# Optimization experiments

Measured on AMD Instinct MI355X. Metric: run time of the kernel, lower is better.

The kernel has to match this reference:

```python
import jax, jax.numpy as jnp
import numpy as np

DIM = 192
NUM_HEADS = 8
EPS = 1e-12  # F.normalize default eps


def setup_inputs() -> dict:
    key = jax.random.key(0)
    ks = jax.random.split(key, 6)
    b, c, h, w = 8, DIM, 128, 128
    scale = 1.0 / np.sqrt(DIM)  # conv2d default init scale (approx)
    return {
        "input": jax.random.normal(ks[0], (b, c, h, w), dtype=jnp.float32),
        "color": jax.random.normal(ks[1], (b, c, h, w), dtype=jnp.float32),
        "Wq": jax.random.normal(ks[2], (DIM, DIM), dtype=jnp.float32) * scale,
        "Wk": jax.random.normal(ks[3], (DIM, DIM), dtype=jnp.float32) * scale,
        "Wv": jax.random.normal(ks[4], (DIM, DIM), dtype=jnp.float32) * scale,
        "Wo": jax.random.normal(ks[5], (DIM, DIM), dtype=jnp.float32) * scale,
    }


def _proj(x, W):
    # 1x1 conv (bias=False) == channel GEMM: [b,c,h,w] x [out,c] -> [b,out,h,w]
    return jnp.einsum('bchw,oc->bohw', x, W)


def _l2norm(x):
    n = jnp.sqrt(jnp.sum(x * x, axis=-1, keepdims=True))
    return x / jnp.maximum(n, EPS)


def reference(input, color, Wq, Wk, Wv, Wo):
    b, c, h, w = input.shape
    head = NUM_HEADS
    dh = c // head
    hw = h * w
    # q from color, k/v from input
    q = _proj(color, Wq).reshape(b, head, dh, hw)
    k = _proj(input, Wk).reshape(b, head, dh, hw)
    v = _proj(input, Wv).reshape(b, head, dh, hw)
    q = _l2norm(q)
    k = _l2norm(k)
    # transposed (channel) attention: [b,head,dh,dh]
    attn = jnp.einsum('bhcn,bhdn->bhcd', q, k)
    attn = jax.nn.softmax(attn, axis=-1)
    out = jnp.einsum('bhcd,bhdn->bhcn', attn, v)  # [b,head,dh,hw]
    out = out.reshape(b, c, h, w)
    return _proj(out, Wo)
```

## Files before the change

### kernel.cpp

```cpp
#include <hip/hip_runtime.h>
#include <hip/hip_bf16.h>


typedef __attribute__((ext_vector_type(4))) float f32x4;
typedef __attribute__((ext_vector_type(8))) short short8;

#define MFMA16(a, b, c) __builtin_amdgcn_mfma_f32_16x16x32_bf16((a), (b), (c), 0, 0, 0)

__device__ __forceinline__ unsigned int pack_rne(float a, float b) {
  unsigned int ua = __float_as_uint(a), ub = __float_as_uint(b);
  ua += 0x7fffu + ((ua >> 16) & 1u);
  ub += 0x7fffu + ((ub >> 16) & 1u);
  return (ua >> 16) | (ub & 0xffff0000u);
}
__device__ __forceinline__ unsigned short bf16u_rne(float x) {
  unsigned int u = __float_as_uint(x);
  u += 0x7fffu + ((u >> 16) & 1u);
  return (unsigned short)(u >> 16);
}
union S8U { short8 s; unsigned int u[4]; };
__device__ __forceinline__ short8 load_cvt8(const float* p) {
  f32x4 x = *(const f32x4*)p;
  f32x4 y = *(const f32x4*)(p + 4);
  S8U r;
  r.u[0] = pack_rne(x[0], x[1]);
  r.u[1] = pack_rne(x[2], x[3]);
  r.u[2] = pack_rne(y[0], y[1]);
  r.u[3] = pack_rne(y[2], y[3]);
  return r.s;
}

#define HW 16384
#define CDIM 192
#define NB 8
#define GSZ (CDIM * CDIM)
#define NTILE 300
#define FCHUNK 49152
#define BROW 80

__global__ void k0_wvt(const float* __restrict__ Wv, unsigned short* __restrict__ WvT) {
  int idx = blockIdx.x * 256 + threadIdx.x;
  if (idx < CDIM * CDIM) {
    int j = idx / CDIM, cp = idx % CDIM;
    WvT[idx] = bf16u_rne(Wv[(size_t)cp * CDIM + j]);
  }
}

__device__ __forceinline__ short8 bfrag(const char* buf, int row, int lg) {
  return *(const short8*)(buf + row * BROW + lg * 16);
}

__device__ __forceinline__ void stageF(const float* __restrict__ ib,
                                       const float* __restrict__ cb, int c0,
                                       char* fdst, int wave, int lane) {
#pragma unroll
  for (int i = 0; i < 4; ++i) {
    const int instr = wave * 4 + i;
    const int tensor = instr >= 24;
    const int rl = (instr - (tensor ? 24 : 0)) * 8 + (lane >> 3);
    const float* T = tensor ? cb : ib;
    const float* g = T + (size_t)rl * HW + c0 + (lane & 7) * 4;
    __builtin_amdgcn_global_load_lds(
        (const __attribute__((address_space(1))) void*)g,
        (__attribute__((address_space(3))) void*)(fdst + instr * 1024), 16, 0, 0);
  }
}

template <int W>
__device__ __forceinline__ void pair_step(const char* bb, f32x4 (&acc)[25],
                                          int l15, int lg) {
  const short8 aT = bfrag(bb, W * 16 + l15, lg);
  const short8 aB = bfrag(bb, (23 - W) * 16 + l15, lg);
#pragma unroll
  for (int ct = W; ct < 24; ++ct) {
    const short8 b = bfrag(bb, ct * 16 + l15, lg);
    acc[ct - W] = MFMA16(aT, b, acc[ct - W]);
    if (ct >= 23 - W) acc[ct + 1] = MFMA16(aB, b, acc[ct + 1]);
  }
}

__device__ __forceinline__ void pair_dispatch(int wave, const char* bb,
                                              f32x4 (&acc)[25], int l15, int lg) {
  switch (wave) {
    case 0: pair_step<0>(bb, acc, l15, lg); break;
    case 1: pair_step<1>(bb, acc, l15, lg); break;
    case 2: pair_step<2>(bb, acc, l15, lg); break;
    case 3: pair_step<3>(bb, acc, l15, lg); break;
    case 4: pair_step<4>(bb, acc, l15, lg); break;
    case 5: pair_step<5>(bb, acc, l15, lg); break;
    case 6: pair_step<6>(bb, acc, l15, lg); break;
    case 7: pair_step<7>(bb, acc, l15, lg); break;
    case 8: pair_step<8>(bb, acc, l15, lg); break;
    case 9: pair_step<9>(bb, acc, l15, lg); break;
    case 10: pair_step<10>(bb, acc, l15, lg); break;
    default: pair_step<11>(bb, acc, l15, lg); break;
  }
}

__global__ __launch_bounds__(768) void gram2_k(const float* __restrict__ input,
                                               const float* __restrict__ color,
                                               float* __restrict__ part,
                                               int npart, int cpb) {
  __shared__ __align__(16) char fbuf[2][FCHUNK];
  __shared__ __align__(16) char bbuf[384 * BROW];
  const int tid = threadIdx.x, wave = tid >> 6, lane = tid & 63;
  const int l15 = lane & 15, lg = (lane >> 4) & 3;
  const int strip = blockIdx.x, b = blockIdx.y;
  const float* ib = input + (size_t)b * CDIM * HW;
  const float* cb = color + (size_t)b * CDIM * HW;
  const int cbase = strip * cpb;

  f32x4 acc[25];
#pragma unroll
  for (int i = 0; i < 25; ++i) acc[i] = (f32x4){0.f, 0.f, 0.f, 0.f};

  stageF(ib, cb, cbase * 32, fbuf[0], wave, lane);
#pragma unroll 1
  for (int c = 0; c < cpb; ++c) {
    if (c + 1 < cpb) {
      stageF(ib, cb, (cbase + c + 1) * 32, fbuf[(c + 1) & 1], wave, lane);
      asm volatile("s_waitcnt vmcnt(4)" ::: "memory");
    } else {
      asm volatile("s_waitcnt vmcnt(0)" ::: "memory");
    }
    __builtin_amdgcn_sched_barrier(0);
    __builtin_amdgcn_s_barrier();
    {
      const char* fb = fbuf[c & 1];
#pragma unroll
      for (int u0 = 0; u0 < 2; ++u0) {
        const int u = tid + u0 * 768;
        const int zr = u >> 2, sub = u & 3;
        const char* src = fb + zr * 128 + sub * 32;
        f32x4 x = *(const f32x4*)src;
        f32x4 y = *(const f32x4*)(src + 16);
        S8U pk;
        pk.u[0] = pack_rne(x[0], x[1]);
        pk.u[1] = pack_rne(x[2], x[3]);
        pk.u[2] = pack_rne(y[0], y[1]);
        pk.u[3] = pack_rne(y[2], y[3]);
        *(short8*)(bbuf + zr * BROW + sub * 16) = pk.s;
      }
    }
    asm volatile("s_waitcnt lgkmcnt(0)" ::: "memory");
    __builtin_amdgcn_sched_barrier(0);
    __builtin_amdgcn_s_barrier();
    pair_dispatch(wave, bbuf, acc, l15, lg);
  }

  float* pbase = part + (size_t)(b * npart + strip) * NTILE * 256;
#pragma unroll
  for (int s = 0; s < 25; ++s)
    *(f32x4*)(pbase + ((size_t)(wave * 25 + s) * 64 + lane) * 4) = acc[s];
}

template <int NP>
__global__ __launch_bounds__(256) void reduce_k(const float* __restrict__ part,
                                                float* __restrict__ G) {
  const int b = blockIdx.y;
  const int T = blockIdx.x * 4 + (threadIdx.x >> 6);
  const int lane = threadIdx.x & 63;
  const float* p = part + ((size_t)b * NP * NTILE + T) * 256 + lane * 4;
  f32x4 v[NP];
#pragma unroll
  for (int s = 0; s < NP; ++s) v[s] = *(const f32x4*)(p + (size_t)s * NTILE * 256);
  f32x4 sum = v[0];
#pragma unroll
  for (int s = 1; s < NP; ++s) {
    sum[0] += v[s][0]; sum[1] += v[s][1]; sum[2] += v[s][2]; sum[3] += v[s][3];
  }
  const int w = T / 25, s = T % 25;
  int rt, ct;
  if (s <= 23 - w) { rt = w; ct = w + s; }
  else { rt = 23 - w; ct = s - 1; }
  int type, gm, gn;
  if (ct < 12) { type = 2; gm = rt; gn = ct; }
  else if (rt < 12) { type = 0; gm = rt; gn = ct - 12; }
  else { type = 1; gm = rt - 12; gn = ct - 12; }
  float* Gm = G + ((size_t)type * NB + b) * GSZ;
  const int l15 = lane & 15, lg = lane >> 4;
  const int row0 = gm * 16 + lg * 4, col = gn * 16 + l15;
#pragma unroll
  for (int r = 0; r < 4; ++r) Gm[(size_t)(row0 + r) * CDIM + col] = sum[r];
  if (type != 0 && rt != ct) {
#pragma unroll
    for (int r = 0; r < 4; ++r) Gm[(size_t)col * CDIM + (row0 + r)] = sum[r];
  }
}

__global__ __launch_bounds__(256) void k2a(const float* __restrict__ G,
                                           const float* __restrict__ Wq,
                                           const float* __restrict__ Wk,
                                           float* __restrict__ A_pre,
                                           float* __restrict__ nqk) {
  const int b = blockIdx.x, type = blockIdx.y;
  __shared__ __align__(16) unsigned short Hs[192][200];
  const int tid = threadIdx.x, wave = tid >> 6, lane = tid & 63;
  const int l15 = lane & 15, lg = lane >> 4, row0 = wave * 48;
  const float* W1 = (type == 2) ? Wk : Wq;
  const float* Gm = G + ((size_t)type * NB + b) * GSZ;

  f32x4 acc[3][12];
#pragma unroll
  for (int t = 0; t < 3; t++)
#pragma unroll
    for (int j = 0; j < 12; j++) acc[t][j] = (f32x4){0.f, 0.f, 0.f, 0.f};

  for (int ks = 0; ks < 192; ks += 32) {
    short8 afr[3];
#pragma unroll
    for (int t = 0; t < 3; t++)
      afr[t] = load_cvt8(W1 + (size_t)(row0 + t * 16 + l15) * CDIM + ks + lg * 8);
#pragma unroll
    for (int tj = 0; tj < 12; tj++) {
      short8 bfr = load_cvt8(Gm + (size_t)(tj * 16 + l15) * CDIM + ks + lg * 8);
#pragma unroll
      for (int t = 0; t < 3; t++) acc[t][tj] = MFMA16(afr[t], bfr, acc[t][tj]);
    }
  }
#pragma unroll
  for (int t = 0; t < 3; t++)
#pragma unroll
    for (int tj = 0; tj < 12; tj++)
#pragma unroll
      for (int r = 0; r < 4; r++)
        Hs[row0 + t * 16 + lg * 4 + r][tj * 16 + l15] = bf16u_rne(acc[t][tj][r]);
  __syncthreads();

  if (type == 0) {
    f32x4 a2[3][12];
#pragma unroll
    for (int t = 0; t < 3; t++)
#pragma unroll
      for (int j = 0; j < 12; j++) a2[t][j] = (f32x4){0.f, 0.f, 0.f, 0.f};
    for (int ks = 0; ks < 192; ks += 32) {
      short8 afr[3];
#pragma unroll
      for (int t = 0; t < 3; t++)
        afr[t] = *(const short8*)&Hs[row0 + t * 16 + l15][ks + lg * 8];
#pragma unroll
      for (int tj = 0; tj < 12; tj++) {
        short8 bfr = load_cvt8(Wk + (size_t)(tj * 16 + l15) * CDIM + ks + lg * 8);
#pragma unroll
        for (int t = 0; t < 3; t++) a2[t][tj] = MFMA16(afr[t], bfr, a2[t][tj]);
      }
    }
    float* Ab = A_pre + (size_t)b * GSZ;
#pragma unroll
    for (int t = 0; t < 3; t++)
#pragma unroll
      for (int tj = 0; tj < 12; tj++)
#pragma unroll
        for (int r = 0; r < 4; r++)
          Ab[(size_t)(row0 + t * 16 + lg * 4 + r) * CDIM + tj * 16 + l15] = a2[t][tj][r];
  } else {
    f32x4 a2[3];
#pragma unroll
    for (int t = 0; t < 3; t++) a2[t] = (f32x4){0.f, 0.f, 0.f, 0.f};
    for (int ks = 0; ks < 192; ks += 32) {
#pragma unroll
      for (int t = 0; t < 3; t++) {
        short8 afr = *(const short8*)&Hs[row0 + t * 16 + l15][ks + lg * 8];
        short8 bfr = load_cvt8(W1 + (size_t)(row0 + t * 16 + l15) * CDIM + ks + lg * 8);
        a2[t] = MFMA16(afr, bfr, a2[t]);
      }
    }
    float* dst = nqk + ((size_t)(type - 1) * NB + b) * CDIM;
#pragma unroll
    for (int t = 0; t < 3; t++)
#pragma unroll
      for (int r = 0; r < 4; r++)
        if (lg * 4 + r == l15) dst[row0 + t * 16 + l15] = a2[t][r];
  }
}

__global__ void k2b(const float* __restrict__ A_pre, const float* __restrict__ nqk,
                    float* __restrict__ attnw) {
  const int b = blockIdx.x, tid = threadIdx.x;
  const int h = tid >> 5, r = tid & 31;
  if (r >= 24) return;
  const float* Ab = A_pre + (size_t)b * GSZ;
  const float* nq = nqk + (size_t)b * CDIM;
  const float* nk = nqk + (size_t)(NB + b) * CDIM;
  const int c = h * 24 + r;
  const float qn = rsqrtf(fmaxf(nq[c], 1e-24f));
  float e[24];
  float mx = -1e30f;
#pragma unroll
  for (int d = 0; d < 24; d++) {
    float kn = rsqrtf(fmaxf(nk[h * 24 + d], 1e-24f));
    float l = Ab[(size_t)c * CDIM + h * 24 + d] * qn * kn;
    e[d] = l;
    mx = fmaxf(mx, l);
  }
  float s = 0.f;
#pragma unroll
  for (int d = 0; d < 24; d++) {
    float x = __expf(e[d] - mx);
    e[d] = x;
    s += x;
  }
  const float inv = 1.0f / s;
  float* dst = attnw + (((size_t)b * NB + h) * 24 + r) * 24;
#pragma unroll
  for (int d = 0; d < 24; d++) dst[d] = e[d] * inv;
}

__global__ __launch_bounds__(256) void k3(const float* __restrict__ attnw,
                                          const float* __restrict__ Wo,
                                          const unsigned short* __restrict__ WvT,
                                          unsigned short* __restrict__ Pbf) {
  const int b = blockIdx.x;
  __shared__ __align__(16) unsigned short AT[192][200];
  __shared__ __align__(16) unsigned short Ms[192][200];
  const int tid = threadIdx.x, wave = tid >> 6, lane = tid & 63;
  const int l15 = lane & 15, lg = lane >> 4, row0 = wave * 48;

  unsigned int* ATu = (unsigned int*)&AT[0][0];
  for (int i = tid; i < 192 * 100; i += 256) ATu[i] = 0u;
  __syncthreads();
  const float* at = attnw + (size_t)b * NB * 24 * 24;
  for (int i = tid; i < 4608; i += 256) {
    int h = i / 576, rem = i % 576, c = rem / 24, d = rem % 24;
    AT[h * 24 + d][h * 24 + c] = bf16u_rne(at[(h * 24 + c) * 24 + d]);
  }
  __syncthreads();

  f32x4 acc[3][12];
#pragma unroll
  for (int t = 0; t < 3; t++)
#pragma unroll
    for (int j = 0; j < 12; j++) acc[t][j] = (f32x4){0.f, 0.f, 0.f, 0.f};
  for (int ks = 0; ks < 192; ks += 32) {
    short8 afr[3];
#pragma unroll
    for (int t = 0; t < 3; t++)
      afr[t] = load_cvt8(Wo + (size_t)(row0 + t * 16 + l15) * CDIM + ks + lg * 8);
#pragma unroll
    for (int tj = 0; tj < 12; tj++) {
      short8 bfr = *(const short8*)&AT[tj * 16 + l15][ks + lg * 8];
#pragma unroll
      for (int t = 0; t < 3; t++) acc[t][tj] = MFMA16(afr[t], bfr, acc[t][tj]);
    }
  }
#pragma unroll
  for (int t = 0; t < 3; t++)
#pragma unroll
    for (int tj = 0; tj < 12; tj++)
#pragma unroll
      for (int r = 0; r < 4; r++)
        Ms[row0 + t * 16 + lg * 4 + r][tj * 16 + l15] = bf16u_rne(acc[t][tj][r]);
  __syncthreads();

  f32x4 a2[3][12];
#pragma unroll
  for (int t = 0; t < 3; t++)
#pragma unroll
    for (int j = 0; j < 12; j++) a2[t][j] = (f32x4){0.f, 0.f, 0.f, 0.f};
  for (int ks = 0; ks < 192; ks += 32) {
    short8 afr[3];
#pragma unroll
    for (int t = 0; t < 3; t++)
      afr[t] = *(const short8*)&Ms[row0 + t * 16 + l15][ks + lg * 8];
#pragma unroll
    for (int tj = 0; tj < 12; tj++) {
      short8 bfr = *(const short8*)(WvT + (size_t)(tj * 16 + l15) * CDIM + ks + lg * 8);
#pragma unroll
      for (int t = 0; t < 3; t++) a2[t][tj] = MFMA16(afr[t], bfr, a2[t][tj]);
    }
  }
  unsigned short* Pb = Pbf + (size_t)b * GSZ;
#pragma unroll
  for (int t = 0; t < 3; t++)
#pragma unroll
    for (int tj = 0; tj < 12; tj++)
#pragma unroll
      for (int r = 0; r < 4; r++)
        Pb[(size_t)(row0 + t * 16 + lg * 4 + r) * CDIM + tj * 16 + l15] = bf16u_rne(a2[t][tj][r]);
}

__global__ __launch_bounds__(256) void kD(const unsigned short* __restrict__ Pbf,
                                          const float* __restrict__ input,
                                          float* __restrict__ out) {
  const int nchunk = blockIdx.x, b = blockIdx.y;
  const int n0 = nchunk * 128;
  __shared__ __align__(16) char BsT[128 * 384];
  const int tid = threadIdx.x, wave = tid >> 6, lane = tid & 63;
  const int l15 = lane & 15, lg = lane >> 4, row0 = wave * 48;

  {
    const int n4 = (tid & 31) * 4;
    const int kb0 = (tid >> 5) * 4;
    const float* src = input + (size_t)b * CDIM * HW + n0 + n4;
    f32x4 w[24];
#pragma unroll
    for (int rnd = 0; rnd < 6; ++rnd)
#pragma unroll
      for (int j = 0; j < 4; ++j)
        w[rnd * 4 + j] = *(const f32x4*)(src + (size_t)(kb0 + rnd * 32 + j) * HW);
    __builtin_amdgcn_sched_barrier(0);
    char* bsb = BsT;
#pragma unroll
    for (int rnd = 0; rnd < 6; ++rnd) {
      const int kb = kb0 + rnd * 32;
#pragma unroll
      for (int i = 0; i < 4; ++i) {
        const int n = n4 + i;
        unsigned long long pk =
            (unsigned long long)pack_rne(w[rnd * 4 + 0][i], w[rnd * 4 + 1][i]) |
            ((unsigned long long)pack_rne(w[rnd * 4 + 2][i], w[rnd * 4 + 3][i]) << 32);
        *(unsigned long long*)(bsb + n * 384 + ((kb * 2) ^ ((n & 7) << 4))) = pk;
      }
    }
  }
  __syncthreads();

  f32x4 acc[3][8];
#pragma unroll
  for (int t = 0; t < 3; t++)
#pragma unroll
    for (int j = 0; j < 8; j++) acc[t][j] = (f32x4){0.f, 0.f, 0.f, 0.f};

  const unsigned short* Pb = Pbf + (size_t)b * GSZ;
#pragma unroll 2
  for (int ks = 0; ks < 6; ks++) {
    short8 afr[3];
#pragma unroll
    for (int t = 0; t < 3; t++)
      afr[t] = *(const short8*)(Pb + (size_t)(row0 + t * 16 + l15) * CDIM + ks * 32 + lg * 8);
#pragma unroll
    for (int tn = 0; tn < 8; tn++) {
      const int n = tn * 16 + l15;
      short8 bfr = *(const short8*)(BsT + n * 384 + ((ks * 64 + lg * 16) ^ ((n & 7) << 4)));
#pragma unroll
      for (int t = 0; t < 3; t++) acc[t][tn] = MFMA16(afr[t], bfr, acc[t][tn]);
    }
  }
  float* ob = out + (size_t)b * CDIM * HW + n0;
#pragma unroll
  for (int t = 0; t < 3; t++)
#pragma unroll
    for (int tn = 0; tn < 8; tn++)
#pragma unroll
      for (int r = 0; r < 4; r++) {
        const int m = row0 + t * 16 + lg * 4 + r;
        ob[(size_t)m * HW + tn * 16 + l15] = acc[t][tn][r];
      }
}

extern "C" void kernel_launch(void* const* d_in, const int* in_sizes, int n_in,
                              void* d_out, int out_size, void* d_ws, size_t ws_size,
                              hipStream_t stream) {
  const float* input = (const float*)d_in[0];
  const float* color = (const float*)d_in[1];
  const float* Wq = (const float*)d_in[2];
  const float* Wk = (const float*)d_in[3];
  const float* Wv = (const float*)d_in[4];
  const float* Wo = (const float*)d_in[5];
  float* out = (float*)d_out;
  char* ws = (char*)d_ws;

  const size_t OFF_G = 0;
  const size_t OFF_APRE = 3538944;
  const size_t OFF_NQK = OFF_APRE + 1179648;
  const size_t OFF_ATT = OFF_NQK + 12288;
  const size_t OFF_WVT = OFF_ATT + 147456;
  const size_t OFF_PBF = OFF_WVT + 73728;
  const size_t OFF_PART = OFF_PBF + 589824;

  float* G = (float*)(ws + OFF_G);
  float* A_pre = (float*)(ws + OFF_APRE);
  float* nqk = (float*)(ws + OFF_NQK);
  float* attnw = (float*)(ws + OFF_ATT);
  unsigned short* WvT = (unsigned short*)(ws + OFF_WVT);
  unsigned short* Pbf = (unsigned short*)(ws + OFF_PBF);
  float* part = (float*)(ws + OFF_PART);

  int npart = 32;
  while (npart > 2 && OFF_PART + (size_t)npart * NB * NTILE * 1024 > ws_size) npart >>= 1;
  const int cpb = 512 / npart;

  k0_wvt<<<dim3(144), dim3(256), 0, stream>>>(Wv, WvT);
  gram2_k<<<dim3(npart, NB), dim3(768), 0, stream>>>(input, color, part, npart, cpb);
  switch (npart) {
    case 32: reduce_k<32><<<dim3(75, NB), dim3(256), 0, stream>>>(part, G); break;
    case 16: reduce_k<16><<<dim3(75, NB), dim3(256), 0, stream>>>(part, G); break;
    case 8:  reduce_k<8><<<dim3(75, NB), dim3(256), 0, stream>>>(part, G); break;
    case 4:  reduce_k<4><<<dim3(75, NB), dim3(256), 0, stream>>>(part, G); break;
    default: reduce_k<2><<<dim3(75, NB), dim3(256), 0, stream>>>(part, G); break;
  }
  k2a<<<dim3(NB, 3), dim3(256), 0, stream>>>(G, Wq, Wk, A_pre, nqk);
  k2b<<<dim3(NB), dim3(256), 0, stream>>>(A_pre, nqk, attnw);
  k3<<<dim3(NB), dim3(256), 0, stream>>>(attnw, Wo, WvT, Pbf);
  kD<<<dim3(HW / 128, NB), dim3(256), 0, stream>>>(Pbf, input, out);
}
```

Measured before the change: 203.5 us.

## Deepen gram staging pipeline to four 16-column slots with prefetch after barrier

The Gram kernel now splits each 32-column chunk into two 16-column slots (64-byte row segments) held in a four-slot LDS ring. It prefetches two chunks ahead, issuing those loads after the conversion barrier so the slots being overwritten are no longer read. The aim is to keep more global loads in flight and hide memory latency behind the MFMA work. The cost is shorter contiguous row segments per load and a vmcnt(4) wait that now relies on the new issue order.

```diff
diff --git a/kernel.cpp b/kernel.cpp
--- a/kernel.cpp
+++ b/kernel.cpp
@@ -35,7 +35,7 @@
 #define NB 8
 #define GSZ (CDIM * CDIM)
 #define NTILE 300
-#define FCHUNK 49152
+#define FSLOT 24576
 #define BROW 80
 
 __global__ void k0_wvt(const float* __restrict__ Wv, unsigned short* __restrict__ WvT) {
@@ -50,19 +50,19 @@
   return *(const short8*)(buf + row * BROW + lg * 16);
 }
 
-__device__ __forceinline__ void stageF(const float* __restrict__ ib,
-                                       const float* __restrict__ cb, int c0,
+__device__ __forceinline__ void stageC(const float* __restrict__ ib,
+                                       const float* __restrict__ cb, int col0,
                                        char* fdst, int wave, int lane) {
 #pragma unroll
-  for (int i = 0; i < 4; ++i) {
-    const int instr = wave * 4 + i;
-    const int tensor = instr >= 24;
-    const int rl = (instr - (tensor ? 24 : 0)) * 8 + (lane >> 3);
+  for (int i = 0; i < 2; ++i) {
+    const int g = wave * 2 + i;
+    const int tensor = g >= 12;
+    const int row = (g - (tensor ? 12 : 0)) * 16 + (lane >> 2);
     const float* T = tensor ? cb : ib;
-    const float* g = T + (size_t)rl * HW + c0 + (lane & 7) * 4;
+    const float* gp = T + (size_t)row * HW + col0 + (lane & 3) * 4;
     __builtin_amdgcn_global_load_lds(
-        (const __attribute__((address_space(1))) void*)g,
-        (__attribute__((address_space(3))) void*)(fdst + instr * 1024), 16, 0, 0);
+        (const __attribute__((address_space(1))) void*)gp,
+        (__attribute__((address_space(3))) void*)(fdst + g * 1024), 16, 0, 0);
   }
 }
 
@@ -100,25 +100,28 @@
 __global__ __launch_bounds__(768) void gram2_k(const float* __restrict__ input,
                                                const float* __restrict__ color,
                                                float* __restrict__ part,
-                                               int npart, int cpb) {
-  __shared__ __align__(16) char fbuf[2][FCHUNK];
+                                               int npart, int ncp) {
+  __shared__ __align__(16) char fbuf[4][FSLOT];
   __shared__ __align__(16) char bbuf[384 * BROW];
   const int tid = threadIdx.x, wave = tid >> 6, lane = tid & 63;
   const int l15 = lane & 15, lg = (lane >> 4) & 3;
   const int strip = blockIdx.x, b = blockIdx.y;
   const float* ib = input + (size_t)b * CDIM * HW;
   const float* cb = color + (size_t)b * CDIM * HW;
-  const int cbase = strip * cpb;
+  const int ch0 = strip * ncp * 2;
 
   f32x4 acc[25];
 #pragma unroll
   for (int i = 0; i < 25; ++i) acc[i] = (f32x4){0.f, 0.f, 0.f, 0.f};
 
-  stageF(ib, cb, cbase * 32, fbuf[0], wave, lane);
+  stageC(ib, cb, (ch0 + 0) * 16, fbuf[0], wave, lane);
+  stageC(ib, cb, (ch0 + 1) * 16, fbuf[1], wave, lane);
+  stageC(ib, cb, (ch0 + 2) * 16, fbuf[2], wave, lane);
+  stageC(ib, cb, (ch0 + 3) * 16, fbuf[3], wave, lane);
+
 #pragma unroll 1
-  for (int c = 0; c < cpb; ++c) {
-    if (c + 1 < cpb) {
-      stageF(ib, cb, (cbase + c + 1) * 32, fbuf[(c + 1) & 1], wave, lane);
+  for (int cp = 0; cp < ncp; ++cp) {
+    if (cp + 1 < ncp) {
       asm volatile("s_waitcnt vmcnt(4)" ::: "memory");
     } else {
       asm volatile("s_waitcnt vmcnt(0)" ::: "memory");
@@ -126,12 +129,13 @@
     __builtin_amdgcn_sched_barrier(0);
     __builtin_amdgcn_s_barrier();
     {
-      const char* fb = fbuf[c & 1];
+      const char* sA = fbuf[(2 * cp) & 3];
+      const char* sB = fbuf[(2 * cp + 1) & 3];
 #pragma unroll
       for (int u0 = 0; u0 < 2; ++u0) {
         const int u = tid + u0 * 768;
         const int zr = u >> 2, sub = u & 3;
-        const char* src = fb + zr * 128 + sub * 32;
+        const char* src = (sub < 2 ? sA : sB) + zr * 64 + (sub & 1) * 32;
         f32x4 x = *(const f32x4*)src;
         f32x4 y = *(const f32x4*)(src + 16);
         S8U pk;
@@ -145,6 +149,10 @@
     asm volatile("s_waitcnt lgkmcnt(0)" ::: "memory");
     __builtin_amdgcn_sched_barrier(0);
     __builtin_amdgcn_s_barrier();
+    if (cp + 2 < ncp) {
+      stageC(ib, cb, (ch0 + 2 * cp + 4) * 16, fbuf[(2 * cp + 4) & 3], wave, lane);
+      stageC(ib, cb, (ch0 + 2 * cp + 5) * 16, fbuf[(2 * cp + 5) & 3], wave, lane);
+    }
     pair_dispatch(wave, bbuf, acc, l15, lg);
   }
 
@@ -478,10 +486,10 @@
 
   int npart = 32;
   while (npart > 2 && OFF_PART + (size_t)npart * NB * NTILE * 1024 > ws_size) npart >>= 1;
-  const int cpb = 512 / npart;
+  const int ncp = 512 / npart;
 
   k0_wvt<<<dim3(144), dim3(256), 0, stream>>>(Wv, WvT);
-  gram2_k<<<dim3(npart, NB), dim3(768), 0, stream>>>(input, color, part, npart, cpb);
+  gram2_k<<<dim3(npart, NB), dim3(768), 0, stream>>>(input, color, part, npart, ncp);
   switch (npart) {
     case 32: reduce_k<32><<<dim3(75, NB), dim3(256), 0, stream>>>(part, G); break;
     case 16: reduce_k<16><<<dim3(75, NB), dim3(256), 0, stream>>>(part, G); break;
```

Result: faster. 198.7 us (-2.4%).
